# Performance work log

Hardware: AMD Instinct MI355X
Metric: run time of the kernel (lower is better)

The kernel has to match this reference:

```python
import jax, jax.numpy as jnp
import numpy as np
import math

D_MODEL = 256
NUM_HEADS = 8
D_HEAD = D_MODEL // NUM_HEADS


def setup_inputs() -> dict:
    key = jax.random.key(0)
    k1, k2, k3, k4, k5 = jax.random.split(key, 5)
    B, T, N = 8, 32, 256
    x = jax.random.normal(k1, (B, T, N, D_MODEL), dtype=jnp.float32)
    boxes_in_flat = jax.random.uniform(k2, (B * T * N, 4), dtype=jnp.float32)
    s = 1.0 / math.sqrt(D_MODEL)
    W_Q = jax.random.uniform(k3, (D_MODEL, D_MODEL), jnp.float32, -s, s)
    W_K = jax.random.uniform(k4, (D_MODEL, D_MODEL), jnp.float32, -s, s)
    W_V = jax.random.uniform(k5, (D_MODEL, D_MODEL), jnp.float32, -s, s)
    return {"x": x, "boxes_in_flat": boxes_in_flat, "W_Q": W_Q, "W_K": W_K, "W_V": W_V}


def reference(x, boxes_in_flat, W_Q, W_K, W_V):
    # x: [B, T, N, D]; boxes_in_flat is unused by the original forward.
    B, T, N, D = x.shape
    H, dh = NUM_HEADS, D_HEAD
    # Temporal attention pooling: softmax over T, weighted sum over T.
    t_w = jax.nn.softmax(x, axis=1)              # [B,T,N,D]
    TAtt = jnp.sum(x * t_w, axis=1)              # [B,N,D] (original tiles this over T; identical values)
    # QKV projections (nn.Linear without bias: y = x @ W^T).
    Q = (x @ W_Q.T).reshape(B, T, N, H, dh)      # [B,T,N,H,dh]
    K = (TAtt @ W_K.T).reshape(B, N, H, dh)      # [B,N,H,dh]
    V = (TAtt @ W_V.T).reshape(B, N, H, dh)      # [B,N,H,dh]
    # ReLU-scored attention with added self-loop (identity), no softmax.
    A = jnp.einsum('btnhd,bmhd->bthnm', Q, K) / jnp.sqrt(jnp.asarray(dh, x.dtype))
    A = jax.nn.relu(A) + jnp.eye(N, dtype=x.dtype)  # [B,T,H,N,N]
    out = jnp.einsum('bthnm,bmhd->btnhd', A, V)     # [B,T,N,H,dh]
    return out.reshape(B, T, N, H * dh)
```

## Files before the change

### kernel.cpp

```cpp
#include <hip/hip_runtime.h>
#include <hip/hip_bf16.h>

#define BB 8
#define TT 32
#define NN 256
#define DD 256
#define HH 8
#define DH 32

typedef __attribute__((ext_vector_type(8))) short short8v;
typedef __attribute__((ext_vector_type(4))) float f32x4;
typedef __attribute__((ext_vector_type(16))) float f32x16;
typedef __attribute__((ext_vector_type(2))) unsigned int u32x2;

static __device__ __forceinline__ unsigned short f2bfu(float f) {
    __hip_bfloat16 h = __float2bfloat16(f);
    unsigned short u;
    __builtin_memcpy(&u, &h, 2);
    return u;
}
static __device__ __forceinline__ unsigned int pkbf(float a, float b) {
    float2 f2; f2.x = a; f2.y = b;
    __hip_bfloat162 h2 = __float22bfloat162_rn(f2);
    unsigned int u;
    __builtin_memcpy(&u, &h2, 4);
    return u;
}

__global__ __launch_bounds__(256) void wfrag_kernel(const float* __restrict__ Wq,
                                                    const float* __restrict__ Wk,
                                                    const float* __restrict__ Wv,
                                                    short* __restrict__ Wf) {
    int bid = blockIdx.x;
    int mat = bid >> 4, ctile = bid & 15;
    const float* W = (mat == 0) ? Wq : (mat == 1) ? Wk : Wv;
    short* out = Wf + (size_t)mat * (16 * 8 * 64 * 8) + (size_t)ctile * (8 * 64 * 8);
    int tid = threadIdx.x;
    int kc = tid >> 5, kg = (tid >> 3) & 3, j = tid & 7;
#pragma unroll
    for (int i = 0; i < 16; ++i) {
        float v = W[(size_t)(ctile * 16 + i) * DD + tid];
        int lane = i | (kg << 4);
        out[((size_t)kc * 64 + lane) * 8 + j] = (short)f2bfu(v);
    }
}

__global__ __launch_bounds__(256) void tatt_kernel(const float* __restrict__ x,
                                                   float* __restrict__ tatt) {
    int gid = blockIdx.x * 256 + threadIdx.x;
    int b = gid >> 16;
    int rem = gid & 0xFFFF;
    const float* xp = x + (size_t)b * TT * NN * DD + rem;
    float vals[TT];
    float mx = -3.0e38f;
#pragma unroll
    for (int t = 0; t < TT; ++t) {
        vals[t] = xp[(size_t)t * (NN * DD)];
        mx = fmaxf(mx, vals[t]);
    }
    float se = 0.f, wsum = 0.f;
#pragma unroll
    for (int t = 0; t < TT; ++t) {
        float e = __expf(vals[t] - mx);
        se += e;
        wsum += e * vals[t];
    }
    tatt[gid] = wsum / se;
}

__global__ __launch_bounds__(256) void kv_kernel(const float* __restrict__ tatt,
                                                 const short* __restrict__ Wkf,
                                                 const short* __restrict__ Wvf,
                                                 short* __restrict__ Kf,
                                                 short* __restrict__ Vf) {
    __shared__ short Xb[64][264];
    int row0 = blockIdx.x * 64;
    int tid = threadIdx.x;

#pragma unroll
    for (int i = 0; i < 16; ++i) {
        int f = i * 256 + tid;
        int rr = f >> 6;
        int c4 = f & 63;
        float4 xv = *(const float4*)(tatt + (size_t)(row0 + rr) * DD + c4 * 4);
        short4 sv;
        sv.x = (short)f2bfu(xv.x);
        sv.y = (short)f2bfu(xv.y);
        sv.z = (short)f2bfu(xv.z);
        sv.w = (short)f2bfu(xv.w);
        *(short4*)&Xb[rr][c4 * 4] = sv;
    }
    __syncthreads();

    int w = tid >> 6, l = tid & 63;
    int lg = l >> 4, lr = l & 15;
    const f32x4 zero = {0.f, 0.f, 0.f, 0.f};

#pragma unroll
    for (int mat = 0; mat < 2; ++mat) {
        const short* Wfm = mat ? Wvf : Wkf;
#pragma unroll
        for (int ct = 0; ct < 4; ++ct) {
            int c = ct * 64 + w * 16 + lr;
            int ctile = ct * 4 + w;
            short8v bf[8];
#pragma unroll
            for (int kc = 0; kc < 8; ++kc)
                bf[kc] = *(const short8v*)(Wfm + (((size_t)ctile * 8 + kc) * 64 + l) * 8);
            int h = c >> 5, kap = c & 31;
#pragma unroll
            for (int rt4 = 0; rt4 < 4; ++rt4) {
                f32x4 acc = zero;
#pragma unroll
                for (int kc = 0; kc < 8; ++kc) {
                    short8v a = *(const short8v*)&Xb[rt4 * 16 + lr][kc * 32 + lg * 8];
                    acc = __builtin_amdgcn_mfma_f32_16x16x32_bf16(a, bf[kc], acc, 0, 0, 0);
                }
#pragma unroll
                for (int r = 0; r < 4; ++r) {
                    int row = row0 + rt4 * 16 + lg * 4 + r;
                    int b = row >> 8, n = row & 255;
                    if (mat == 0) {
                        float val = acc[r] * 0.17677669529663688f;
                        size_t o = ((((size_t)(b * HH + h) * 8 + (n >> 5)) * 2 + (kap >> 4)) * 64
                                    + (n & 31) + 32 * ((kap >> 3) & 1)) * 8 + (kap & 7);
                        Kf[o] = (short)f2bfu(val);
                    } else {
                        int d = kap;
                        size_t o = ((((size_t)(b * HH + h) * 8 + (n >> 5)) * 2 + ((n >> 4) & 1)) * 64
                                    + d + 32 * ((n >> 3) & 1)) * 8 + (n & 7);
                        Vf[o] = (short)f2bfu(acc[r]);
                    }
                }
            }
        }
    }
}

__global__ __launch_bounds__(256) void qproj_kernel(const float* __restrict__ x,
                                                    const short* __restrict__ Wqf,
                                                    short* __restrict__ Qb) {
    __shared__ short Xb[64][264];
    int row0 = blockIdx.x * 64;
    int tid = threadIdx.x;

#pragma unroll
    for (int i = 0; i < 16; ++i) {
        int f = i * 256 + tid;
        int rr = f >> 6;
        int c4 = f & 63;
        float4 xv = *(const float4*)(x + (size_t)(row0 + rr) * DD + c4 * 4);
        short4 sv;
        sv.x = (short)f2bfu(xv.x);
        sv.y = (short)f2bfu(xv.y);
        sv.z = (short)f2bfu(xv.z);
        sv.w = (short)f2bfu(xv.w);
        *(short4*)&Xb[rr][c4 * 4] = sv;
    }
    __syncthreads();

    int w = tid >> 6, l = tid & 63;
    int lg = l >> 4, lr = l & 15;
    const f32x4 zero = {0.f, 0.f, 0.f, 0.f};

#pragma unroll
    for (int ct = 0; ct < 4; ++ct) {
        int c = ct * 64 + w * 16 + lr;
        int ctile = ct * 4 + w;
        short8v bf[8];
#pragma unroll
        for (int kc = 0; kc < 8; ++kc)
            bf[kc] = *(const short8v*)(Wqf + (((size_t)ctile * 8 + kc) * 64 + l) * 8);
        int h = c >> 5, kap = c & 31;
#pragma unroll
        for (int rt4 = 0; rt4 < 4; ++rt4) {
            f32x4 acc = zero;
#pragma unroll
            for (int kc = 0; kc < 8; ++kc) {
                short8v a = *(const short8v*)&Xb[rt4 * 16 + lr][kc * 32 + lg * 8];
                acc = __builtin_amdgcn_mfma_f32_16x16x32_bf16(a, bf[kc], acc, 0, 0, 0);
            }
#pragma unroll
            for (int r = 0; r < 4; ++r) {
                int row = row0 + rt4 * 16 + lg * 4 + r;
                int b = row >> 13;
                int t = (row >> 8) & 31;
                int n = row & 255;
                size_t o = (((((size_t)(b * TT + t) * HH + h) * 8 + (n >> 5)) * 2 + (kap >> 4)) * 64
                            + (n & 31) + 32 * ((kap >> 3) & 1)) * 8 + (kap & 7);
                Qb[o] = (short)f2bfu(acc[r]);
            }
        }
    }
}

__global__ __launch_bounds__(256, 4) void attn_kernel(const short* __restrict__ Qf,
                                                      const short* __restrict__ Kf,
                                                      const short* __restrict__ Vf,
                                                      float* __restrict__ out) {
    int bid = blockIdx.x;
    int h = bid & 7;
    int t = (bid >> 3) & 31;
    int b = bid >> 8;
    int tid = threadIdx.x;
    int w = tid >> 6, l = tid & 63;
    int pos = l & 31, hi = l >> 5;

    const short8v* qp = (const short8v*)Qf + ((size_t)bid * 8 + 2 * w) * 2 * 64 + l;
    short8v qf00 = qp[0];
    short8v qf01 = qp[64];
    short8v qf10 = qp[128];
    short8v qf11 = qp[192];

    const short8v* kp = (const short8v*)Kf + (size_t)(b * HH + h) * 16 * 64 + l;
    const short8v* vp = (const short8v*)Vf + (size_t)(b * HH + h) * 16 * 64 + l;

    const f32x16 z16 = {};
    f32x16 o0 = z16, o1 = z16;

#pragma unroll 2
    for (int mt = 0; mt < 8; ++mt) {
        short8v kf0 = kp[mt * 128];
        short8v kf1 = kp[mt * 128 + 64];
        short8v vf0 = vp[mt * 128];
        short8v vf1 = vp[mt * 128 + 64];
#pragma unroll
        for (int qi = 0; qi < 2; ++qi) {
            short8v qa = qi ? qf10 : qf00;
            short8v qb = qi ? qf11 : qf01;
            f32x16 p = __builtin_amdgcn_mfma_f32_32x32x16_bf16(kf0, qa, z16, 0, 0, 0);
            p = __builtin_amdgcn_mfma_f32_32x32x16_bf16(kf1, qb, p, 0, 0, 0);
#pragma unroll
            for (int r = 0; r < 16; ++r) p[r] = fmaxf(p[r], 0.f);
            if (mt == 2 * w + qi) {
#pragma unroll
                for (int r = 0; r < 16; ++r) {
                    int mloc = (r & 3) + 8 * (r >> 2) + 4 * hi;
                    if (mloc == pos) p[r] += 1.f;
                }
            }
#pragma unroll
            for (int c = 0; c < 2; ++c) {
                unsigned int A0 = pkbf(p[8 * c + 0], p[8 * c + 1]);
                unsigned int A1 = pkbf(p[8 * c + 2], p[8 * c + 3]);
                unsigned int B0 = pkbf(p[8 * c + 4], p[8 * c + 5]);
                unsigned int B1 = pkbf(p[8 * c + 6], p[8 * c + 7]);
                u32x2 s0 = __builtin_amdgcn_permlane32_swap(A0, B0, false, false);
                u32x2 s1 = __builtin_amdgcn_permlane32_swap(A1, B1, false, false);
                union { unsigned int u[4]; short8v s; } pa;
                pa.u[0] = s0[0];
                pa.u[1] = s1[0];
                pa.u[2] = s0[1];
                pa.u[3] = s1[1];
                short8v vv = c ? vf1 : vf0;
                if (qi == 0)
                    o0 = __builtin_amdgcn_mfma_f32_32x32x16_bf16(pa.s, vv, o0, 0, 0, 0);
                else
                    o1 = __builtin_amdgcn_mfma_f32_32x32x16_bf16(pa.s, vv, o1, 0, 0, 0);
            }
        }
    }

    float* ob = out + ((size_t)(b * TT + t) * NN) * DD + h * DH + pos;
#pragma unroll
    for (int r = 0; r < 16; ++r) {
        int mloc = (r & 3) + 8 * (r >> 2) + 4 * hi;
        ob[(size_t)((2 * w + 0) * 32 + mloc) * DD] = o0[r];
        ob[(size_t)((2 * w + 1) * 32 + mloc) * DD] = o1[r];
    }
}

extern "C" void kernel_launch(void* const* d_in, const int* in_sizes, int n_in,
                              void* d_out, int out_size, void* d_ws, size_t ws_size,
                              hipStream_t stream) {
    (void)in_sizes; (void)n_in; (void)out_size; (void)ws_size;
    const float* x  = (const float*)d_in[0];
    const float* Wq = (const float*)d_in[2];
    const float* Wk = (const float*)d_in[3];
    const float* Wv = (const float*)d_in[4];
    float* out = (float*)d_out;

    char* base = (char*)d_ws;
    float* tatt = (float*)base;
    short* Kfp = (short*)(base + (size_t)2 * 1024 * 1024);
    short* Vfp = (short*)(base + (size_t)3 * 1024 * 1024);
    short* Qbp = (short*)(base + (size_t)4 * 1024 * 1024);
    short* Wf  = (short*)(base + (size_t)36 * 1024 * 1024);
    short* Wqf = Wf;
    short* Wkf = Wf + (size_t)16 * 8 * 64 * 8;
    short* Wvf = Wkf + (size_t)16 * 8 * 64 * 8;

    wfrag_kernel<<<48, 256, 0, stream>>>(Wq, Wk, Wv, Wf);
    tatt_kernel<<<(BB * NN * DD) / 256, 256, 0, stream>>>(x, tatt);
    kv_kernel<<<BB * NN / 64, 256, 0, stream>>>(tatt, Wkf, Wvf, Kfp, Vfp);
    qproj_kernel<<<BB * TT * NN / 64, 256, 0, stream>>>(x, Wqf, Qbp);
    attn_kernel<<<BB * TT * HH, 256, 0, stream>>>(Qbp, Kfp, Vfp, out);
}
```

Before: 180.3 us.

## Fuse temporal pooling, Q projection and K/V projection into one kernel

Replaces the separate temporal-softmax, K/V projection and Q projection kernels with one kernel. Each 1024-thread block owns one batch and 8 tokens. It streams all 32 time steps of x once through shared memory, accumulating the temporal softmax sums and computing Q along the way, then runs K/V on the pooled rows. This removes the second full read of x and the fp32 pooling buffer round-trip through global memory. In exchange, the pooling now uses bf16-rounded inputs without max subtraction, which risks accuracy loss and overflow. The grid is also only 256 large blocks at one block per CU, so latency hiding is limited.

```diff
diff --git a/kernel.cpp b/kernel.cpp
--- a/kernel.cpp
+++ b/kernel.cpp
@@ -25,6 +25,11 @@
     unsigned int u;
     __builtin_memcpy(&u, &h2, 4);
     return u;
+}
+static __device__ __forceinline__ float bfu2f(unsigned int ubits) {
+    union { unsigned int u; float f; } c;
+    c.u = ubits << 16;
+    return c.f;
 }
 
 __global__ __launch_bounds__(256) void wfrag_kernel(const float* __restrict__ Wq,
@@ -45,150 +50,118 @@
     }
 }
 
-__global__ __launch_bounds__(256) void tatt_kernel(const float* __restrict__ x,
-                                                   float* __restrict__ tatt) {
-    int gid = blockIdx.x * 256 + threadIdx.x;
-    int b = gid >> 16;
-    int rem = gid & 0xFFFF;
-    const float* xp = x + (size_t)b * TT * NN * DD + rem;
-    float vals[TT];
-    float mx = -3.0e38f;
-#pragma unroll
-    for (int t = 0; t < TT; ++t) {
-        vals[t] = xp[(size_t)t * (NN * DD)];
-        mx = fmaxf(mx, vals[t]);
-    }
-    float se = 0.f, wsum = 0.f;
-#pragma unroll
-    for (int t = 0; t < TT; ++t) {
-        float e = __expf(vals[t] - mx);
-        se += e;
-        wsum += e * vals[t];
-    }
-    tatt[gid] = wsum / se;
-}
-
-__global__ __launch_bounds__(256) void kv_kernel(const float* __restrict__ tatt,
-                                                 const short* __restrict__ Wkf,
-                                                 const short* __restrict__ Wvf,
-                                                 short* __restrict__ Kf,
-                                                 short* __restrict__ Vf) {
+__global__ __launch_bounds__(1024, 1) void fused_tqkv_kernel(
+        const float* __restrict__ x,
+        const short* __restrict__ Wqf,
+        const short* __restrict__ Wkf,
+        const short* __restrict__ Wvf,
+        short* __restrict__ Qb,
+        short* __restrict__ Kf,
+        short* __restrict__ Vf) {
     __shared__ short Xb[64][264];
-    int row0 = blockIdx.x * 64;
+    int bid = blockIdx.x;
+    int b = bid >> 5;
+    int n0 = (bid & 31) * 8;
     int tid = threadIdx.x;
-
-#pragma unroll
-    for (int i = 0; i < 16; ++i) {
-        int f = i * 256 + tid;
-        int rr = f >> 6;
-        int c4 = f & 63;
-        float4 xv = *(const float4*)(tatt + (size_t)(row0 + rr) * DD + c4 * 4);
-        short4 sv;
-        sv.x = (short)f2bfu(xv.x);
-        sv.y = (short)f2bfu(xv.y);
-        sv.z = (short)f2bfu(xv.z);
-        sv.w = (short)f2bfu(xv.w);
-        *(short4*)&Xb[rr][c4 * 4] = sv;
-    }
-    __syncthreads();
-
     int w = tid >> 6, l = tid & 63;
     int lg = l >> 4, lr = l & 15;
     const f32x4 zero = {0.f, 0.f, 0.f, 0.f};
 
-#pragma unroll
-    for (int mat = 0; mat < 2; ++mat) {
-        const short* Wfm = mat ? Wvf : Wkf;
-#pragma unroll
-        for (int ct = 0; ct < 4; ++ct) {
-            int c = ct * 64 + w * 16 + lr;
-            int ctile = ct * 4 + w;
-            short8v bf[8];
-#pragma unroll
-            for (int kc = 0; kc < 8; ++kc)
-                bf[kc] = *(const short8v*)(Wfm + (((size_t)ctile * 8 + kc) * 64 + l) * 8);
-            int h = c >> 5, kap = c & 31;
-#pragma unroll
-            for (int rt4 = 0; rt4 < 4; ++rt4) {
-                f32x4 acc = zero;
-#pragma unroll
-                for (int kc = 0; kc < 8; ++kc) {
-                    short8v a = *(const short8v*)&Xb[rt4 * 16 + lr][kc * 32 + lg * 8];
-                    acc = __builtin_amdgcn_mfma_f32_16x16x32_bf16(a, bf[kc], acc, 0, 0, 0);
-                }
-#pragma unroll
-                for (int r = 0; r < 4; ++r) {
-                    int row = row0 + rt4 * 16 + lg * 4 + r;
-                    int b = row >> 8, n = row & 255;
-                    if (mat == 0) {
-                        float val = acc[r] * 0.17677669529663688f;
-                        size_t o = ((((size_t)(b * HH + h) * 8 + (n >> 5)) * 2 + (kap >> 4)) * 64
-                                    + (n & 31) + 32 * ((kap >> 3) & 1)) * 8 + (kap & 7);
-                        Kf[o] = (short)f2bfu(val);
-                    } else {
-                        int d = kap;
-                        size_t o = ((((size_t)(b * HH + h) * 8 + (n >> 5)) * 2 + ((n >> 4) & 1)) * 64
-                                    + d + 32 * ((n >> 3) & 1)) * 8 + (n & 7);
-                        Vf[o] = (short)f2bfu(acc[r]);
-                    }
-                }
-            }
-        }
-    }
-}
-
-__global__ __launch_bounds__(256) void qproj_kernel(const float* __restrict__ x,
-                                                    const short* __restrict__ Wqf,
-                                                    short* __restrict__ Qb) {
-    __shared__ short Xb[64][264];
-    int row0 = blockIdx.x * 64;
-    int tid = threadIdx.x;
-
-#pragma unroll
-    for (int i = 0; i < 16; ++i) {
-        int f = i * 256 + tid;
-        int rr = f >> 6;
-        int c4 = f & 63;
-        float4 xv = *(const float4*)(x + (size_t)(row0 + rr) * DD + c4 * 4);
-        short4 sv;
-        sv.x = (short)f2bfu(xv.x);
-        sv.y = (short)f2bfu(xv.y);
-        sv.z = (short)f2bfu(xv.z);
-        sv.w = (short)f2bfu(xv.w);
-        *(short4*)&Xb[rr][c4 * 4] = sv;
-    }
-    __syncthreads();
-
-    int w = tid >> 6, l = tid & 63;
-    int lg = l >> 4, lr = l & 15;
-    const f32x4 zero = {0.f, 0.f, 0.f, 0.f};
-
-#pragma unroll
-    for (int ct = 0; ct < 4; ++ct) {
-        int c = ct * 64 + w * 16 + lr;
-        int ctile = ct * 4 + w;
-        short8v bf[8];
-#pragma unroll
-        for (int kc = 0; kc < 8; ++kc)
-            bf[kc] = *(const short8v*)(Wqf + (((size_t)ctile * 8 + kc) * 64 + l) * 8);
-        int h = c >> 5, kap = c & 31;
+    int c = w * 16 + lr;
+    int h = c >> 5, kap = c & 31;
+    short8v bq[8];
+#pragma unroll
+    for (int kc = 0; kc < 8; ++kc)
+        bq[kc] = *(const short8v*)(Wqf + (((size_t)w * 8 + kc) * 64 + l) * 8);
+
+    int tn = tid >> 7;
+    int td = (tid & 127) * 2;
+    float se0 = 0.f, ws0 = 0.f, se1 = 0.f, ws1 = 0.f;
+
+    for (int tc = 0; tc < 4; ++tc) {
+        __syncthreads();
+#pragma unroll
+        for (int i = 0; i < 4; ++i) {
+            int f = i * 1024 + tid;
+            int rr = f >> 6, c4 = f & 63;
+            int t = tc * 8 + (rr >> 3), n = n0 + (rr & 7);
+            float4 xv = *(const float4*)(x + ((size_t)(b * TT + t) * NN + n) * DD + c4 * 4);
+            short4 sv;
+            sv.x = (short)f2bfu(xv.x);
+            sv.y = (short)f2bfu(xv.y);
+            sv.z = (short)f2bfu(xv.z);
+            sv.w = (short)f2bfu(xv.w);
+            *(short4*)&Xb[rr][c4 * 4] = sv;
+        }
+        __syncthreads();
+
+#pragma unroll
+        for (int tt = 0; tt < 8; ++tt) {
+            unsigned int pr = *(const unsigned int*)&Xb[tt * 8 + tn][td];
+            float v0 = bfu2f(pr & 0xFFFFu);
+            float v1 = bfu2f(pr >> 16);
+            float e0 = __expf(v0);
+            float e1 = __expf(v1);
+            se0 += e0; ws0 += v0 * e0;
+            se1 += e1; ws1 += v1 * e1;
+        }
+
 #pragma unroll
         for (int rt4 = 0; rt4 < 4; ++rt4) {
             f32x4 acc = zero;
 #pragma unroll
             for (int kc = 0; kc < 8; ++kc) {
                 short8v a = *(const short8v*)&Xb[rt4 * 16 + lr][kc * 32 + lg * 8];
-                acc = __builtin_amdgcn_mfma_f32_16x16x32_bf16(a, bf[kc], acc, 0, 0, 0);
+                acc = __builtin_amdgcn_mfma_f32_16x16x32_bf16(a, bq[kc], acc, 0, 0, 0);
             }
 #pragma unroll
             for (int r = 0; r < 4; ++r) {
-                int row = row0 + rt4 * 16 + lg * 4 + r;
-                int b = row >> 13;
-                int t = (row >> 8) & 31;
-                int n = row & 255;
+                int rowloc = rt4 * 16 + lg * 4 + r;
+                int t = tc * 8 + (rowloc >> 3);
+                int n = n0 + (rowloc & 7);
                 size_t o = (((((size_t)(b * TT + t) * HH + h) * 8 + (n >> 5)) * 2 + (kap >> 4)) * 64
                             + (n & 31) + 32 * ((kap >> 3) & 1)) * 8 + (kap & 7);
                 Qb[o] = (short)f2bfu(acc[r]);
+            }
+        }
+    }
+
+    __syncthreads();
+    {
+        float t0 = ws0 / se0;
+        float t1 = ws1 / se1;
+        *(unsigned int*)&Xb[tn][td] = pkbf(t0, t1);
+        *(unsigned int*)&Xb[tn + 8][td] = 0u;
+    }
+    __syncthreads();
+
+#pragma unroll
+    for (int mat = 0; mat < 2; ++mat) {
+        const short* Wfm = mat ? Wvf : Wkf;
+        short8v bfr[8];
+#pragma unroll
+        for (int kc = 0; kc < 8; ++kc)
+            bfr[kc] = *(const short8v*)(Wfm + (((size_t)w * 8 + kc) * 64 + l) * 8);
+        f32x4 acc = zero;
+#pragma unroll
+        for (int kc = 0; kc < 8; ++kc) {
+            short8v a = *(const short8v*)&Xb[lr][kc * 32 + lg * 8];
+            acc = __builtin_amdgcn_mfma_f32_16x16x32_bf16(a, bfr[kc], acc, 0, 0, 0);
+        }
+        if (lg < 2) {
+#pragma unroll
+            for (int r = 0; r < 4; ++r) {
+                int n = n0 + lg * 4 + r;
+                if (mat == 0) {
+                    float val = acc[r] * 0.17677669529663688f;
+                    size_t o = ((((size_t)(b * HH + h) * 8 + (n >> 5)) * 2 + (kap >> 4)) * 64
+                                + (n & 31) + 32 * ((kap >> 3) & 1)) * 8 + (kap & 7);
+                    Kf[o] = (short)f2bfu(val);
+                } else {
+                    size_t o = ((((size_t)(b * HH + h) * 8 + (n >> 5)) * 2 + ((n >> 4) & 1)) * 64
+                                + kap + 32 * ((n >> 3) & 1)) * 8 + (n & 7);
+                    Vf[o] = (short)f2bfu(acc[r]);
+                }
             }
         }
     }
@@ -281,18 +254,15 @@
     float* out = (float*)d_out;
 
     char* base = (char*)d_ws;
-    float* tatt = (float*)base;
-    short* Kfp = (short*)(base + (size_t)2 * 1024 * 1024);
-    short* Vfp = (short*)(base + (size_t)3 * 1024 * 1024);
-    short* Qbp = (short*)(base + (size_t)4 * 1024 * 1024);
-    short* Wf  = (short*)(base + (size_t)36 * 1024 * 1024);
+    short* Kfp = (short*)base;
+    short* Vfp = (short*)(base + (size_t)1 * 1024 * 1024);
+    short* Qbp = (short*)(base + (size_t)2 * 1024 * 1024);
+    short* Wf  = (short*)(base + (size_t)34 * 1024 * 1024);
     short* Wqf = Wf;
     short* Wkf = Wf + (size_t)16 * 8 * 64 * 8;
     short* Wvf = Wkf + (size_t)16 * 8 * 64 * 8;
 
     wfrag_kernel<<<48, 256, 0, stream>>>(Wq, Wk, Wv, Wf);
-    tatt_kernel<<<(BB * NN * DD) / 256, 256, 0, stream>>>(x, tatt);
-    kv_kernel<<<BB * NN / 64, 256, 0, stream>>>(tatt, Wkf, Wvf, Kfp, Vfp);
-    qproj_kernel<<<BB * TT * NN / 64, 256, 0, stream>>>(x, Wqf, Qbp);
+    fused_tqkv_kernel<<<BB * 32, 1024, 0, stream>>>(x, Wqf, Wkf, Wvf, Qbp, Kfp, Vfp);
     attn_kernel<<<BB * TT * HH, 256, 0, stream>>>(Qbp, Kfp, Vfp, out);
 }
```

New measurement: 158.4 us. 1.14x faster.
